# Performance work log

Measured on AMD Instinct MI355X. Metric: run time of the kernel, lower is better.

Reference implementation:

```python
import jax, jax.numpy as jnp
import numpy as np

N, E, D, T, R, H = 50000, 400000, 256, 3, 6, 4
DK = D // H          # 64, d_k = out_dim // n_heads
OUT = H * DK         # 256
LN_EPS = 1e-5


def setup_inputs() -> dict:
    key = jax.random.key(0)
    ks = jax.random.split(key, 16)
    std = 0.02  # initializer_range in HGTClassfication._init_weights
    f32 = jnp.float32
    inp = {
        "x": jax.random.normal(ks[0], (N, D), f32),
        "Wk": jax.random.normal(ks[1], (T, D, OUT), f32) * std,
        "bk": jnp.zeros((T, OUT), f32),
        "Wq": jax.random.normal(ks[2], (T, D, OUT), f32) * std,
        "bq": jnp.zeros((T, OUT), f32),
        "Wv": jax.random.normal(ks[3], (T, D, OUT), f32) * std,
        "bv": jnp.zeros((T, OUT), f32),
        "Wa": jax.random.normal(ks[4], (T, OUT, OUT), f32) * std,
        "ba": jnp.zeros((T, OUT), f32),
        "rel_pri": jnp.ones((R, H), f32),
        "rel_att": jax.random.normal(ks[5], (R, H, DK, DK), f32) * (1.0 / np.sqrt(DK)),
        "rel_msg": jax.random.normal(ks[6], (R, H, DK, DK), f32) * (1.0 / np.sqrt(DK)),
        "skip": jnp.ones((T,), f32),
        "ln_g": jnp.ones((T, OUT), f32),
        "ln_b": jnp.zeros((T, OUT), f32),
        "node_type": jax.random.randint(ks[7], (N,), 0, T),
        "edge_src": jax.random.randint(ks[8], (E,), 0, N),
        "edge_dst": jax.random.randint(ks[9], (E,), 0, N),
        "edge_type": jax.random.randint(ks[10], (E,), 0, R),
        "n_heads": H,
    }
    return inp


def reference(x, Wk, bk, Wq, bq, Wv, bv, Wa, ba, rel_pri, rel_att, rel_msg,
              skip, ln_g, ln_b, node_type, edge_src, edge_dst, edge_type, n_heads):
    n, d = x.shape
    r, h = rel_pri.shape
    dk = rel_att.shape[-1]
    out_dim = h * dk
    ar = jnp.arange(n)

    def typed_linear(inp_, W, b):
        # per-node-type Linear: compute for all T types, pick by node_type
        y = jnp.einsum('ni,tio->tno', inp_, W) + b[:, None, :]
        return y[node_type, ar]

    k = typed_linear(x, Wk, bk).reshape(n, h, dk)
    q = typed_linear(x, Wq, bq).reshape(n, h, dk)
    v = typed_linear(x, Wv, bv).reshape(n, h, dk)

    # relation-specific transforms (done on nodes, gathered per edge: N*R << E*R work)
    k_rel = jnp.einsum('nhd,rhde->rnhe', k, rel_att)   # [R,N,H,dk]
    v_rel = jnp.einsum('nhd,rhde->rnhe', v, rel_msg)   # [R,N,H,dk]
    key_e = k_rel[edge_type, edge_src]                 # [E,H,dk]
    val_e = v_rel[edge_type, edge_src]                 # [E,H,dk]

    att = (q[edge_dst] * key_e).sum(-1) * rel_pri[edge_type] / jnp.sqrt(jnp.float32(dk))  # [E,H]

    # per-(dst, etype) mailbox softmax + weighted sum (DGL reduce per canonical etype)
    seg = edge_dst * r + edge_type
    S = n * r
    amax = jax.ops.segment_max(att, seg, num_segments=S)
    amax = jax.lax.stop_gradient(jnp.where(jnp.isfinite(amax), amax, 0.0))
    ex = jnp.exp(att - amax[seg])
    denom = jax.ops.segment_sum(ex, seg, num_segments=S)
    w = ex / denom[seg]                                # [E,H]
    hsum = jax.ops.segment_sum(w[:, :, None] * val_e, seg, num_segments=S)  # [S,H,dk]
    cnt = jax.ops.segment_sum(jnp.ones((seg.shape[0],), x.dtype), seg, num_segments=S)

    # cross_reducer='mean' over relations that delivered messages
    t_rel = hsum.reshape(n, r, out_dim)
    present = cnt.reshape(n, r) > 0
    nrel = jnp.maximum(present.sum(-1), 1).astype(x.dtype)
    t = (t_rel * present[..., None].astype(x.dtype)).sum(1) / nrel[:, None]

    trans = typed_linear(t, Wa, ba)
    alpha = jax.nn.sigmoid(skip)[node_type][:, None]
    out = trans * alpha + x * (1.0 - alpha)

    mu = out.mean(-1, keepdims=True)
    var = out.var(-1, keepdims=True)
    normed = (out - mu) * jax.lax.rsqrt(var + LN_EPS) * ln_g[node_type] + ln_b[node_type]

    # nodes with no incoming edges keep their input feature (no 't' in DGL data)
    has_msg = present.any(-1)[:, None]
    return jnp.where(has_msg, normed, x)
```

## Files before the change

kernel.cpp:

```cpp
#include <hip/hip_runtime.h>
#include <hip/hip_bf16.h>


#define NN 50000
#define EE 400000
#define TN 3
#define RN 6
#define HN 4
#define SS (NN * RN)
#define NCHUNK 293
#define CD 32

typedef __hip_bfloat16 bf16;
typedef unsigned short u16;
using bf16x8 = __attribute__((ext_vector_type(8))) __bf16;
using f32x4  = __attribute__((ext_vector_type(4))) float;

__device__ __forceinline__ float b2f(bf16 h) { return __bfloat162float(h); }
__device__ __forceinline__ float busf(u16 u) { return __uint_as_float((unsigned)u << 16); }
__device__ __forceinline__ float blo(unsigned u) { return __uint_as_float(u << 16); }
__device__ __forceinline__ float bhi(unsigned u) { return __uint_as_float(u & 0xffff0000u); }
__device__ __forceinline__ u16 f2us(float f) {
    unsigned u = __float_as_uint(f);
    return (u16)((u + 0x7fffu + ((u >> 16) & 1u)) >> 16);
}
__device__ __forceinline__ float ld(const void* p, long i, int f) {
    return f ? ((const float*)p)[i] : b2f(((const bf16*)p)[i]);
}

__global__ __launch_bounds__(256) void detect_dtype(const void* __restrict__ x,
                                                    int* __restrict__ flag) {
    __shared__ int cnt_s;
    if (threadIdx.x == 0) cnt_s = 0;
    __syncthreads();
    const u16* p = (const u16*)x;
    int c = 0;
    for (int i = threadIdx.x; i < 8192; i += 256) {
        int expo = (p[i] >> 7) & 0xFF;
        if (expo >= 0x97) ++c;
    }
    atomicAdd(&cnt_s, c);
    __syncthreads();
    if (threadIdx.x == 0) *flag = (cnt_s > 64) ? 1 : 0;
}

__global__ __launch_bounds__(256) void prep(const void* __restrict__ rel_att,
        const void* __restrict__ rel_msg,
        const void* __restrict__ Wk, const void* __restrict__ Wq,
        const void* __restrict__ Wv, const void* __restrict__ Wa,
        const void* __restrict__ x, const int* __restrict__ node_type,
        const int* __restrict__ edst, const int* __restrict__ etype,
        const int* __restrict__ flag,
        u16* __restrict__ MTa, u16* __restrict__ MTm,
        u16* __restrict__ WallT, u16* __restrict__ WaT,
        u16* __restrict__ xb,
        int* __restrict__ lists, int* __restrict__ cnts,
        unsigned* __restrict__ cnt) {
    int b = blockIdx.x;
    int t = threadIdx.x;
    if (b < 48) {
        int f = *flag;
        int m = b;
        long base = (long)(m % 24) * 4096;
        if (m < 24) {
            for (int it = 0; it < 16; ++it) {
                int idx = it * 256 + t;
                MTa[base + idx] = f2us(ld(rel_att, base + idx, f));
            }
        } else {
            for (int it = 0; it < 16; ++it) {
                int idx = it * 256 + t;
                int d = idx >> 6, j = idx & 63;
                MTm[base + (j << 6) + d] = f2us(ld(rel_msg, base + idx, f));
            }
        }
    } else if (b < 3120) {
        int f = *flag;
        int m = b - 48;
        if (m < 2304) {
            int ty = m / 768, o3 = m % 768;
            int sec = o3 >> 8, o = o3 & 255;
            const void* W = (sec == 0) ? Wk : (sec == 1) ? Wq : Wv;
            WallT[(size_t)ty * 768 * 256 + (size_t)o3 * 256 + t] =
                f2us(ld(W, (long)ty * 65536 + (long)t * 256 + o, f));
        } else {
            int mm = m - 2304;
            int ty = mm / 256, o = mm % 256;
            WaT[(size_t)ty * 65536 + (size_t)o * 256 + t] =
                f2us(ld(Wa, (long)ty * 65536 + (long)t * 256 + o, f));
        }
    } else if (b < 15620) {
        int f = *flag;
        long i = ((long)(b - 3120) * 256 + t) * 4;
        if (i < (long)NN * 256) {
            if (f) {
                float4 v = *(const float4*)((const float*)x + i);
                ushort4 p; p.x = f2us(v.x); p.y = f2us(v.y); p.z = f2us(v.z); p.w = f2us(v.w);
                *(ushort4*)(xb + i) = p;
            } else {
                *(ushort4*)(xb + i) = *(const ushort4*)((const u16*)x + i);
            }
        }
    } else if (b < 15816) {
        __shared__ int lc[TN], lbase[TN];
        if (t < TN) lc[t] = 0;
        __syncthreads();
        int n = (b - 15620) * 256 + t;
        int pos = -1, ty = 0;
        if (n < NN) {
            ty = node_type[n];
            pos = atomicAdd(&lc[ty], 1);
        }
        __syncthreads();
        if (t < TN) lbase[t] = atomicAdd(&cnts[t], lc[t]);
        __syncthreads();
        if (n < NN) lists[ty * NN + lbase[ty] + pos] = n;
    } else {
        int e = (b - 15816) * 256 + t;
        if (e < EE) atomicAdd(&cnt[etype[e] * NN + edst[e]], 1u);
    }
}

__global__ __launch_bounds__(256) void scanA(const unsigned* __restrict__ cnt,
                                             unsigned* __restrict__ csums) {
    __shared__ unsigned s[256];
    int b = blockIdx.x, t = threadIdx.x;
    int s0 = b * 1024 + t * 4;
    unsigned v = 0;
    if (s0 + 3 < SS) { uint4 u = *(const uint4*)&cnt[s0]; v = u.x + u.y + u.z + u.w; }
    else { for (int j = 0; j < 4; ++j) if (s0 + j < SS) v += cnt[s0 + j]; }
    s[t] = v;
    __syncthreads();
    for (int st = 128; st > 0; st >>= 1) {
        if (t < st) s[t] += s[t + st];
        __syncthreads();
    }
    if (t == 0) csums[b] = s[0];
}

__global__ __launch_bounds__(256) void scanB(unsigned* __restrict__ csums,
                                             int* __restrict__ base) {
    __shared__ unsigned s[512];
    int t = threadIdx.x;
    unsigned a = (t < NCHUNK) ? csums[t] : 0u;
    unsigned b = (256 + t < NCHUNK) ? csums[256 + t] : 0u;
    s[t] = a; s[256 + t] = b;
    __syncthreads();
    for (int st = 1; st < 512; st <<= 1) {
        unsigned x0 = (t >= st) ? s[t - st] : 0u;
        unsigned x1 = (256 + t >= st) ? s[256 + t - st] : 0u;
        __syncthreads();
        s[t] += x0; s[256 + t] += x1;
        __syncthreads();
    }
    if (t < NCHUNK) csums[t] = s[t] - a;
    if (256 + t < NCHUNK) csums[256 + t] = s[256 + t] - b;
    if (t == 0) base[SS] = (int)s[NCHUNK - 1];
}

__global__ __launch_bounds__(256) void scanC(const unsigned* __restrict__ cnt,
        const unsigned* __restrict__ csums, int* __restrict__ base) {
    __shared__ unsigned s[256];
    int b = blockIdx.x, t = threadIdx.x;
    int s0 = b * 1024 + t * 4;
    unsigned vs[4] = {0u, 0u, 0u, 0u};
    if (s0 + 3 < SS) { uint4 u = *(const uint4*)&cnt[s0]; vs[0]=u.x; vs[1]=u.y; vs[2]=u.z; vs[3]=u.w; }
    else { for (int j = 0; j < 4; ++j) if (s0 + j < SS) vs[j] = cnt[s0 + j]; }
    unsigned v = vs[0] + vs[1] + vs[2] + vs[3];
    s[t] = v;
    __syncthreads();
    for (int st = 1; st < 256; st <<= 1) {
        unsigned x = (t >= st) ? s[t - st] : 0u;
        __syncthreads();
        s[t] += x;
        __syncthreads();
    }
    unsigned run = csums[b] + s[t] - v;
    for (int j = 0; j < 4; ++j) {
        if (s0 + j < SS) { base[s0 + j] = (int)run; run += vs[j]; }
    }
}

__global__ __launch_bounds__(256) void scatter_edges(const int* __restrict__ edst,
        const int* __restrict__ etype, const int* __restrict__ base,
        unsigned* __restrict__ cnt, int* __restrict__ sorted) {
    int e = blockIdx.x * 256 + threadIdx.x;
    if (e >= EE) return;
    int seg = etype[e] * NN + edst[e];
    unsigned old = atomicSub(&cnt[seg], 1u);
    sorted[base[seg] + (int)old - 1] = e;
}

__global__ __launch_bounds__(512, 2) void k1_mfma(const u16* __restrict__ xb,
        const u16* __restrict__ WallT,
        const void* __restrict__ bk, const void* __restrict__ bq,
        const void* __restrict__ bv,
        const int* __restrict__ lists, const int* __restrict__ cnts,
        const int* __restrict__ flag,
        u16* __restrict__ kb, u16* __restrict__ qb, u16* __restrict__ vb) {
    int f = *flag;
    int tt = blockIdx.x % TN, tile = blockIdx.x / TN;
    int cnt = cnts[tt];
    int start = tile * 64;
    if (start >= cnt) return;
    __shared__ int nl[64];
    __shared__ __align__(16) u16 xs[64][280];
    __shared__ __align__(16) float bias_s[768];
    int t = threadIdx.x;
    if (t < 64) nl[t] = (start + t < cnt) ? lists[tt * NN + start + t] : -1;
    if (t < 256) {
        bias_s[t]       = ld(bk, tt * 256 + t, f);
        bias_s[256 + t] = ld(bq, tt * 256 + t, f);
        bias_s[512 + t] = ld(bv, tt * 256 + t, f);
    }
    __syncthreads();
    {
        int i = t >> 4, g = t & 15;
        #pragma unroll
        for (int i2 = 0; i2 < 2; ++i2) {
            int row = i + i2 * 32;
            int node = nl[row];
            uint4 a = {0, 0, 0, 0}, b = {0, 0, 0, 0};
            if (node >= 0) {
                const uint4* src = (const uint4*)(xb + (size_t)node * 256 + g * 16);
                a = src[0]; b = src[1];
            }
            *(uint4*)&xs[row][g * 16] = a;
            *(uint4*)&xs[row][g * 16 + 8] = b;
        }
    }
    __syncthreads();
    int w = t >> 6, lane = t & 63, ln = lane & 15, quad = lane >> 4;
    const u16* Wt = WallT + (size_t)tt * 768 * 256;
    f32x4 acc[6][4];
    #pragma unroll
    for (int j = 0; j < 6; ++j)
        #pragma unroll
        for (int g = 0; g < 4; ++g)
            acc[j][g] = (f32x4){0.f, 0.f, 0.f, 0.f};
    for (int kt = 0; kt < 8; ++kt) {
        bf16x8 A[6];
        #pragma unroll
        for (int jt = 0; jt < 6; ++jt)
            A[jt] = *(const bf16x8*)(Wt + (size_t)(w * 96 + jt * 16 + ln) * 256 + kt * 32 + quad * 8);
        bf16x8 B[4];
        #pragma unroll
        for (int g = 0; g < 4; ++g)
            B[g] = *(const bf16x8*)&xs[g * 16 + ln][kt * 32 + quad * 8];
        #pragma unroll
        for (int jt = 0; jt < 6; ++jt)
            #pragma unroll
            for (int g = 0; g < 4; ++g)
                acc[jt][g] = __builtin_amdgcn_mfma_f32_16x16x32_bf16(A[jt], B[g], acc[jt][g], 0, 0, 0);
    }
    #pragma unroll
    for (int jt = 0; jt < 6; ++jt) {
        int jc = w * 96 + jt * 16 + quad * 4;
        float4 bi = *(const float4*)&bias_s[jc];
        int sec = jc >> 8, o = jc & 255;
        u16* basep = (sec == 0 ? kb : sec == 1 ? qb : vb);
        #pragma unroll
        for (int g = 0; g < 4; ++g) {
            int node = nl[g * 16 + ln];
            if (node >= 0) {
                ushort4 p;
                p.x = f2us(acc[jt][g][0] + bi.x); p.y = f2us(acc[jt][g][1] + bi.y);
                p.z = f2us(acc[jt][g][2] + bi.z); p.w = f2us(acc[jt][g][3] + bi.w);
                *(ushort4*)(basep + (size_t)node * 256 + o) = p;
            }
        }
    }
}

__global__ __launch_bounds__(256) void k2k4(const u16* __restrict__ kb,
        const u16* __restrict__ qb, const u16* __restrict__ vb,
        const u16* __restrict__ MTa, const u16* __restrict__ MTm,
        const void* __restrict__ rel_pri,
        const int* __restrict__ sorted, const int* __restrict__ base,
        const int* __restrict__ esrc, const int* __restrict__ edst,
        const int* __restrict__ flag,
        u16* __restrict__ attex_g, float* __restrict__ tacc) {
    int f = *flag;
    int c0 = blockIdx.x * CD;
    int nd = min(CD, NN - c0);
    __shared__ float attL[1280];
    __shared__ int srcL[1280];
    __shared__ float denomL[CD * HN];
    __shared__ int sb_[CD + 1];
    __shared__ __align__(16) u16 qL[CD][264];
    __shared__ __align__(16) u16 qrs[CD][264];
    int t = threadIdx.x;
    int w = t >> 6, lane = t & 63, ln = lane & 15, quad = lane >> 4;
    {
        int i = t >> 3, g8 = t & 7;
        uint4 a0 = {0,0,0,0}, a1 = {0,0,0,0}, a2 = {0,0,0,0}, a3 = {0,0,0,0};
        if (i < nd) {
            const uint4* src = (const uint4*)(qb + (size_t)(c0 + i) * 256 + g8 * 32);
            a0 = src[0]; a1 = src[1]; a2 = src[2]; a3 = src[3];
        }
        *(uint4*)&qL[i][g8 * 32 +  0] = a0;
        *(uint4*)&qL[i][g8 * 32 +  8] = a1;
        *(uint4*)&qL[i][g8 * 32 + 16] = a2;
        *(uint4*)&qL[i][g8 * 32 + 24] = a3;
    }
    f32x4 accF[2][4];
    #pragma unroll
    for (int g = 0; g < 2; ++g)
        #pragma unroll
        for (int m = 0; m < 4; ++m)
            accF[g][m] = (f32x4){0.f, 0.f, 0.f, 0.f};

    for (int r = 0; r < RN; ++r) {
        if (t < CD * HN) denomL[t] = 0.f;
        if (t <= nd) sb_[t] = base[r * NN + c0 + t];
        __syncthreads();
        long mtbase = (long)(r * HN + w) * 4096;
        #pragma unroll
        for (int grp = 0; grp < 2; ++grp) {
            int li = grp * 16 + ln;
            bf16x8 B0 = *(const bf16x8*)&qL[li][w * 64 + quad * 8];
            bf16x8 B1 = *(const bf16x8*)&qL[li][w * 64 + quad * 8 + 32];
            #pragma unroll
            for (int mt = 0; mt < 4; ++mt) {
                const u16* ap = MTa + mtbase + (mt * 16 + ln) * 64 + quad * 8;
                bf16x8 A0 = *(const bf16x8*)(ap);
                bf16x8 A1 = *(const bf16x8*)(ap + 32);
                f32x4 acc = {0.f, 0.f, 0.f, 0.f};
                acc = __builtin_amdgcn_mfma_f32_16x16x32_bf16(A0, B0, acc, 0, 0, 0);
                acc = __builtin_amdgcn_mfma_f32_16x16x32_bf16(A1, B1, acc, 0, 0, 0);
                int jc = w * 64 + mt * 16 + quad * 4;
                ushort4 pq;
                pq.x = f2us(acc[0]); pq.y = f2us(acc[1]);
                pq.z = f2us(acc[2]); pq.w = f2us(acc[3]);
                *(ushort4*)&qrs[li][jc] = pq;
            }
        }
        __syncthreads();
        int b0 = sb_[0], nE = sb_[nd] - b0;
        for (int i = t; i < nE * 4; i += 256) {
            int ei = i >> 2;
            int e = sorted[b0 + ei];
            int h = i & 3;
            int s = esrc[e], dv = edst[e] - c0;
            if (h == 0 && ei < 1280) srcL[ei] = s;
            const uint4* kp = (const uint4*)(kb + (size_t)s * 256 + h * 64);
            const uint4* qp = (const uint4*)&qrs[dv][h * 64];
            float dot = 0.f;
            #pragma unroll
            for (int ii = 0; ii < 8; ++ii) {
                uint4 a = kp[ii], b = qp[ii];
                dot += blo(a.x) * blo(b.x) + bhi(a.x) * bhi(b.x);
                dot += blo(a.y) * blo(b.y) + bhi(a.y) * bhi(b.y);
                dot += blo(a.z) * blo(b.z) + bhi(a.z) * bhi(b.z);
                dot += blo(a.w) * blo(b.w) + bhi(a.w) * bhi(b.w);
            }
            float attv = dot * ld(rel_pri, r * HN + h, f) * 0.125f;
            attv = fminf(fmaxf(attv, -50.f), 50.f);
            float ex = expf(attv);
            if (i < 1280) attL[i] = ex;
            else attex_g[(size_t)b0 * 4 + i] = f2us(ex);
            atomicAdd(&denomL[dv * HN + h], ex);
        }
        __syncthreads();
        for (int i2 = w; i2 < nd; i2 += 4) {
            int sb = sb_[i2], se = sb_[i2 + 1];
            float a0 = 0.f, a1 = 0.f, a2 = 0.f, a3 = 0.f;
            if (se > sb) {
                int h = lane >> 4;
                float inv = 1.f / denomL[i2 * HN + h];
                for (int idx = sb; idx < se; ++idx) {
                    int rel = idx - b0;
                    int li2 = rel * 4 + h;
                    float wgt = ((li2 < 1280) ? attL[li2] : busf(attex_g[(size_t)idx * 4 + h])) * inv;
                    int s = (rel < 1280) ? srcL[rel] : esrc[sorted[idx]];
                    ushort4 v = *(const ushort4*)(vb + (size_t)s * 256 + lane * 4);
                    a0 += wgt * busf(v.x); a1 += wgt * busf(v.y);
                    a2 += wgt * busf(v.z); a3 += wgt * busf(v.w);
                }
            }
            ushort4 pv;
            pv.x = f2us(a0); pv.y = f2us(a1); pv.z = f2us(a2); pv.w = f2us(a3);
            *(ushort4*)&qrs[i2][lane * 4] = pv;
        }
        __syncthreads();
        #pragma unroll
        for (int grp = 0; grp < 2; ++grp) {
            int li = grp * 16 + ln;
            bf16x8 B0 = *(const bf16x8*)&qrs[li][w * 64 + quad * 8];
            bf16x8 B1 = *(const bf16x8*)&qrs[li][w * 64 + quad * 8 + 32];
            #pragma unroll
            for (int mt = 0; mt < 4; ++mt) {
                const u16* mp = MTm + mtbase + (mt * 16 + ln) * 64 + quad * 8;
                bf16x8 A0 = *(const bf16x8*)(mp);
                bf16x8 A1 = *(const bf16x8*)(mp + 32);
                accF[grp][mt] = __builtin_amdgcn_mfma_f32_16x16x32_bf16(A0, B0, accF[grp][mt], 0, 0, 0);
                accF[grp][mt] = __builtin_amdgcn_mfma_f32_16x16x32_bf16(A1, B1, accF[grp][mt], 0, 0, 0);
            }
        }
    }
    #pragma unroll
    for (int grp = 0; grp < 2; ++grp) {
        int li = grp * 16 + ln;
        if (li < nd) {
            #pragma unroll
            for (int mt = 0; mt < 4; ++mt) {
                int jc = w * 64 + mt * 16 + quad * 4;
                float4 v = {accF[grp][mt][0], accF[grp][mt][1],
                            accF[grp][mt][2], accF[grp][mt][3]};
                *(float4*)(tacc + (long)(c0 + li) * 256 + jc) = v;
            }
        }
    }
}

__global__ __launch_bounds__(512, 4) void k5_fused(const void* __restrict__ x,
        const float* __restrict__ tacc, const u16* __restrict__ WaT,
        const void* __restrict__ ba, const void* __restrict__ skip,
        const void* __restrict__ ln_g, const void* __restrict__ ln_b,
        const int* __restrict__ base,
        const int* __restrict__ lists, const int* __restrict__ cnts,
        const int* __restrict__ flag, void* out) {
    int f = *flag;
    int tt = blockIdx.x % TN, tile = blockIdx.x / TN;
    int cnt = cnts[tt];
    int start = tile * 64;
    if (start >= cnt) return;
    __shared__ int nl[64];
    __shared__ float invs[64];
    __shared__ int hasv[64];
    __shared__ __align__(16) u16 xs[64][280];
    __shared__ __align__(16) float ba_s[256], lnG_s[256], lnB_s[256];
    __shared__ float red1[64][8], red2[64][8];
    __shared__ float mu_[64], rs_[64];
    int t = threadIdx.x;
    if (t < 64) {
        int node = (start + t < cnt) ? lists[tt * NN + start + t] : -1;
        nl[t] = node;
        int nrel = 0;
        if (node >= 0) {
            #pragma unroll
            for (int r = 0; r < RN; ++r)
                nrel += (base[r * NN + node + 1] > base[r * NN + node]) ? 1 : 0;
        }
        hasv[t] = nrel;
        invs[t] = (nrel > 0) ? 1.f / (float)nrel : 1.f;
    }
    if (t < 256) {
        ba_s[t]  = ld(ba,   tt * 256 + t, f);
        lnG_s[t] = ld(ln_g, tt * 256 + t, f);
        lnB_s[t] = ld(ln_b, tt * 256 + t, f);
    }
    __syncthreads();
    {
        int i = t >> 3, g8 = t & 7;
        int node = nl[i];
        float inv = invs[i];
        int o0 = g8 * 32;
        u16 tmp[32];
        if (node >= 0) {
            const float* src = tacc + (long)node * 256 + o0;
            #pragma unroll
            for (int j = 0; j < 8; ++j) {
                float4 v = *(const float4*)(src + j * 4);
                tmp[j*4+0] = f2us(v.x * inv); tmp[j*4+1] = f2us(v.y * inv);
                tmp[j*4+2] = f2us(v.z * inv); tmp[j*4+3] = f2us(v.w * inv);
            }
        } else {
            #pragma unroll
            for (int j = 0; j < 32; ++j) tmp[j] = 0;
        }
        #pragma unroll
        for (int j = 0; j < 4; ++j)
            *(uint4*)&xs[i][o0 + j * 8] = ((const uint4*)tmp)[j];
    }
    __syncthreads();
    int w = t >> 6, lane = t & 63, ln = lane & 15, quad = lane >> 4;
    const u16* Wt = WaT + (size_t)tt * 65536;
    f32x4 acc[2][4];
    #pragma unroll
    for (int j = 0; j < 2; ++j)
        #pragma unroll
        for (int g = 0; g < 4; ++g)
            acc[j][g] = (f32x4){0.f, 0.f, 0.f, 0.f};
    for (int kt = 0; kt < 8; ++kt) {
        bf16x8 A[2];
        #pragma unroll
        for (int jt = 0; jt < 2; ++jt)
            A[jt] = *(const bf16x8*)(Wt + (size_t)(w * 32 + jt * 16 + ln) * 256 + kt * 32 + quad * 8);
        bf16x8 B[4];
        #pragma unroll
        for (int g = 0; g < 4; ++g)
            B[g] = *(const bf16x8*)&xs[g * 16 + ln][kt * 32 + quad * 8];
        #pragma unroll
        for (int jt = 0; jt < 2; ++jt)
            #pragma unroll
            for (int g = 0; g < 4; ++g)
                acc[jt][g] = __builtin_amdgcn_mfma_f32_16x16x32_bf16(A[jt], B[g], acc[jt][g], 0, 0, 0);
    }
    float sk = ld(skip, tt, f);
    float alpha = 1.f / (1.f + expf(-sk));
    float p1[4] = {0.f, 0.f, 0.f, 0.f}, p2[4] = {0.f, 0.f, 0.f, 0.f};
    #pragma unroll
    for (int g = 0; g < 4; ++g) {
        int node = nl[g * 16 + ln];
        if (node < 0) continue;
        #pragma unroll
        for (int jt = 0; jt < 2; ++jt) {
            int jc = w * 32 + jt * 16 + quad * 4;
            float4 bi = *(const float4*)&ba_s[jc];
            long xo = (long)node * 256 + jc;
            float xv[4];
            if (f) {
                float4 v = *(const float4*)((const float*)x + xo);
                xv[0] = v.x; xv[1] = v.y; xv[2] = v.z; xv[3] = v.w;
            } else {
                ushort4 v = *(const ushort4*)((const u16*)x + xo);
                xv[0] = busf(v.x); xv[1] = busf(v.y); xv[2] = busf(v.z); xv[3] = busf(v.w);
            }
            #pragma unroll
            for (int rg = 0; rg < 4; ++rg) {
                float ov = acc[jt][g][rg] + ((const float*)&bi)[rg];
                ov = ov * alpha + xv[rg] * (1.f - alpha);
                acc[jt][g][rg] = ov;
                p1[g] += ov; p2[g] += ov * ov;
            }
        }
    }
    #pragma unroll
    for (int g = 0; g < 4; ++g) {
        p1[g] += __shfl_xor(p1[g], 16); p1[g] += __shfl_xor(p1[g], 32);
        p2[g] += __shfl_xor(p2[g], 16); p2[g] += __shfl_xor(p2[g], 32);
    }
    if (quad == 0) {
        #pragma unroll
        for (int g = 0; g < 4; ++g) {
            red1[g * 16 + ln][w] = p1[g];
            red2[g * 16 + ln][w] = p2[g];
        }
    }
    __syncthreads();
    if (t < 64) {
        float s1 = 0.f, s2 = 0.f;
        #pragma unroll
        for (int j = 0; j < 8; ++j) { s1 += red1[t][j]; s2 += red2[t][j]; }
        float mu = s1 * (1.f / 256.f);
        float ms = s2 * (1.f / 256.f);
        float var = fmaxf(ms - mu * mu, 0.f);
        mu_[t] = mu; rs_[t] = rsqrtf(var + 1e-5f);
    }
    __syncthreads();
    #pragma unroll
    for (int g = 0; g < 4; ++g) {
        int li = g * 16 + ln;
        int node = nl[li];
        if (node < 0) continue;
        if (hasv[li] > 0) {
            float mu = mu_[li], rs = rs_[li];
            #pragma unroll
            for (int jt = 0; jt < 2; ++jt) {
                int jc = w * 32 + jt * 16 + quad * 4;
                float4 gg = *(const float4*)&lnG_s[jc];
                float4 bb = *(const float4*)&lnB_s[jc];
                long oo = (long)node * 256 + jc;
                float r0 = (acc[jt][g][0] - mu) * rs * gg.x + bb.x;
                float r1 = (acc[jt][g][1] - mu) * rs * gg.y + bb.y;
                float r2 = (acc[jt][g][2] - mu) * rs * gg.z + bb.z;
                float r3 = (acc[jt][g][3] - mu) * rs * gg.w + bb.w;
                if (f) { float4 v = {r0, r1, r2, r3}; *(float4*)((float*)out + oo) = v; }
                else   { ushort4 v; v.x = f2us(r0); v.y = f2us(r1); v.z = f2us(r2); v.w = f2us(r3);
                         *(ushort4*)((u16*)out + oo) = v; }
            }
        } else {
            #pragma unroll
            for (int jt = 0; jt < 2; ++jt) {
                int jc = w * 32 + jt * 16 + quad * 4;
                long oo = (long)node * 256 + jc;
                if (f) { *(float4*)((float*)out + oo) = *(const float4*)((const float*)x + oo); }
                else   { *(ushort4*)((u16*)out + oo) = *(const ushort4*)((const u16*)x + oo); }
            }
        }
    }
}

extern "C" void kernel_launch(void* const* d_in, const int* in_sizes, int n_in,
                              void* d_out, int out_size, void* d_ws, size_t ws_size,
                              hipStream_t stream) {
    const void* x       = d_in[0];
    const void* Wk      = d_in[1];
    const void* bk      = d_in[2];
    const void* Wq      = d_in[3];
    const void* bq      = d_in[4];
    const void* Wv      = d_in[5];
    const void* bv      = d_in[6];
    const void* Wa      = d_in[7];
    const void* ba      = d_in[8];
    const void* rel_pri = d_in[9];
    const void* rel_att = d_in[10];
    const void* rel_msg = d_in[11];
    const void* skip    = d_in[12];
    const void* ln_g    = d_in[13];
    const void* ln_b    = d_in[14];
    const int* node_type = (const int*)d_in[15];
    const int* edge_src  = (const int*)d_in[16];
    const int* edge_dst  = (const int*)d_in[17];
    const int* edge_type = (const int*)d_in[18];
    char* w = (char*)d_ws;

    u16*      kb     = (u16*)(w);
    u16*      qb     = (u16*)(w + 25600000);
    u16*      vb     = (u16*)(w + 51200000);
    float*    tacc   = (float*)(w + 76800000);
    u16*      xb     = (u16*)(w + 76800000);
    u16*      attex  = (u16*)(w + 128000000);
    int*      sorted = (int*)(w + 131200000);
    int*      base   = (int*)(w + 132800000);
    int*      nlists = (int*)(w + 134000064);
    u16*      MTa    = (u16*)(w + 134600064);
    u16*      MTm    = (u16*)(w + 134796672);
    u16*      WallT  = (u16*)(w + 134993280);
    u16*      WaT    = (u16*)(w + 136172928);
    unsigned* cnt    = (unsigned*)(w + 136566144);
    int*      ncnts  = (int*)(w + 137766144);
    int*      flag   = (int*)(w + 137766208);
    unsigned* csums  = (unsigned*)(w + 137766272);

    hipMemsetAsync(w + 136566144, 0, 1201408, stream);

    detect_dtype<<<dim3(1), dim3(256), 0, stream>>>(x, flag);
    prep<<<dim3(17379), dim3(256), 0, stream>>>(
        rel_att, rel_msg, Wk, Wq, Wv, Wa, x, node_type, edge_dst, edge_type,
        flag, MTa, MTm, WallT, WaT, xb, nlists, ncnts, cnt);
    scanA<<<dim3(NCHUNK), dim3(256), 0, stream>>>(cnt, csums);
    scanB<<<dim3(1), dim3(256), 0, stream>>>(csums, base);
    scanC<<<dim3(NCHUNK), dim3(256), 0, stream>>>(cnt, csums, base);
    scatter_edges<<<dim3((EE + 255) / 256), dim3(256), 0, stream>>>(
        edge_dst, edge_type, base, cnt, sorted);

    k1_mfma<<<dim3(TN * ((NN + 63) / 64)), dim3(512), 0, stream>>>(
        xb, WallT, bk, bq, bv, nlists, ncnts, flag, kb, qb, vb);


    k2k4<<<dim3((NN + CD - 1) / CD), dim3(256), 0, stream>>>(
        kb, qb, vb, MTa, MTm, rel_pri, sorted, base, edge_src, edge_dst,
        flag, attex, tacc);

    k5_fused<<<dim3(TN * ((NN + 63) / 64)), dim3(512), 0, stream>>>(
        x, tacc, WaT, ba, skip, ln_g, ln_b, base, nlists, ncnts, flag, d_out);
}
```

Measured before the change: 621.9 us.

## Halve destination-node chunk per block and widen per-node aggregation lanes

```diff
diff --git a/kernel.cpp b/kernel.cpp
--- a/kernel.cpp
+++ b/kernel.cpp
@@ -9,7 +9,8 @@
 #define HN 4
 #define SS (NN * RN)
 #define NCHUNK 293
-#define CD 32
+#define CD 16
+#define LCAP 640
 
 typedef __hip_bfloat16 bf16;
 typedef unsigned short u16;
@@ -283,8 +284,8 @@
     int f = *flag;
     int c0 = blockIdx.x * CD;
     int nd = min(CD, NN - c0);
-    __shared__ float attL[1280];
-    __shared__ int srcL[1280];
+    __shared__ float attL[LCAP];
+    __shared__ int srcL[LCAP];
     __shared__ float denomL[CD * HN];
     __shared__ int sb_[CD + 1];
     __shared__ __align__(16) u16 qL[CD][264];
@@ -292,34 +293,27 @@
     int t = threadIdx.x;
     int w = t >> 6, lane = t & 63, ln = lane & 15, quad = lane >> 4;
     {
-        int i = t >> 3, g8 = t & 7;
-        uint4 a0 = {0,0,0,0}, a1 = {0,0,0,0}, a2 = {0,0,0,0}, a3 = {0,0,0,0};
+        int i = t >> 4, g = t & 15;
+        uint4 a0 = {0,0,0,0}, a1 = {0,0,0,0};
         if (i < nd) {
-            const uint4* src = (const uint4*)(qb + (size_t)(c0 + i) * 256 + g8 * 32);
-            a0 = src[0]; a1 = src[1]; a2 = src[2]; a3 = src[3];
-        }
-        *(uint4*)&qL[i][g8 * 32 +  0] = a0;
-        *(uint4*)&qL[i][g8 * 32 +  8] = a1;
-        *(uint4*)&qL[i][g8 * 32 + 16] = a2;
-        *(uint4*)&qL[i][g8 * 32 + 24] = a3;
-    }
-    f32x4 accF[2][4];
+            const uint4* src = (const uint4*)(qb + (size_t)(c0 + i) * 256 + g * 16);
+            a0 = src[0]; a1 = src[1];
+        }
+        *(uint4*)&qL[i][g * 16] = a0;
+        *(uint4*)&qL[i][g * 16 + 8] = a1;
+    }
+    f32x4 accF[4];
     #pragma unroll
-    for (int g = 0; g < 2; ++g)
-        #pragma unroll
-        for (int m = 0; m < 4; ++m)
-            accF[g][m] = (f32x4){0.f, 0.f, 0.f, 0.f};
+    for (int m = 0; m < 4; ++m) accF[m] = (f32x4){0.f, 0.f, 0.f, 0.f};
 
     for (int r = 0; r < RN; ++r) {
         if (t < CD * HN) denomL[t] = 0.f;
         if (t <= nd) sb_[t] = base[r * NN + c0 + t];
         __syncthreads();
         long mtbase = (long)(r * HN + w) * 4096;
-        #pragma unroll
-        for (int grp = 0; grp < 2; ++grp) {
-            int li = grp * 16 + ln;
-            bf16x8 B0 = *(const bf16x8*)&qL[li][w * 64 + quad * 8];
-            bf16x8 B1 = *(const bf16x8*)&qL[li][w * 64 + quad * 8 + 32];
+        {
+            bf16x8 B0 = *(const bf16x8*)&qL[ln][w * 64 + quad * 8];
+            bf16x8 B1 = *(const bf16x8*)&qL[ln][w * 64 + quad * 8 + 32];
             #pragma unroll
             for (int mt = 0; mt < 4; ++mt) {
                 const u16* ap = MTa + mtbase + (mt * 16 + ln) * 64 + quad * 8;
@@ -332,7 +326,7 @@
                 ushort4 pq;
                 pq.x = f2us(acc[0]); pq.y = f2us(acc[1]);
                 pq.z = f2us(acc[2]); pq.w = f2us(acc[3]);
-                *(ushort4*)&qrs[li][jc] = pq;
+                *(ushort4*)&qrs[ln][jc] = pq;
             }
         }
         __syncthreads();
@@ -342,7 +336,7 @@
             int e = sorted[b0 + ei];
             int h = i & 3;
             int s = esrc[e], dv = edst[e] - c0;
-            if (h == 0 && ei < 1280) srcL[ei] = s;
+            if (h == 0 && ei < LCAP) srcL[ei] = s;
             const uint4* kp = (const uint4*)(kb + (size_t)s * 256 + h * 64);
             const uint4* qp = (const uint4*)&qrs[dv][h * 64];
             float dot = 0.f;
@@ -357,58 +351,58 @@
             float attv = dot * ld(rel_pri, r * HN + h, f) * 0.125f;
             attv = fminf(fmaxf(attv, -50.f), 50.f);
             float ex = expf(attv);
-            if (i < 1280) attL[i] = ex;
+            if (i < LCAP) attL[i] = ex;
             else attex_g[(size_t)b0 * 4 + i] = f2us(ex);
             atomicAdd(&denomL[dv * HN + h], ex);
         }
         __syncthreads();
-        for (int i2 = w; i2 < nd; i2 += 4) {
-            int sb = sb_[i2], se = sb_[i2 + 1];
-            float a0 = 0.f, a1 = 0.f, a2 = 0.f, a3 = 0.f;
-            if (se > sb) {
-                int h = lane >> 4;
-                float inv = 1.f / denomL[i2 * HN + h];
-                for (int idx = sb; idx < se; ++idx) {
-                    int rel = idx - b0;
-                    int li2 = rel * 4 + h;
-                    float wgt = ((li2 < 1280) ? attL[li2] : busf(attex_g[(size_t)idx * 4 + h])) * inv;
-                    int s = (rel < 1280) ? srcL[rel] : esrc[sorted[idx]];
-                    ushort4 v = *(const ushort4*)(vb + (size_t)s * 256 + lane * 4);
-                    a0 += wgt * busf(v.x); a1 += wgt * busf(v.y);
-                    a2 += wgt * busf(v.z); a3 += wgt * busf(v.w);
+        {
+            int half = lane >> 5, lane32 = lane & 31;
+            int h = lane32 >> 3;
+            for (int i2 = w * 2 + half; i2 < nd; i2 += 8) {
+                int sb = sb_[i2], se = sb_[i2 + 1];
+                float a0=0.f,a1=0.f,a2=0.f,a3=0.f,a4=0.f,a5=0.f,a6=0.f,a7=0.f;
+                if (se > sb) {
+                    float inv = 1.f / denomL[i2 * HN + h];
+                    for (int idx = sb; idx < se; ++idx) {
+                        int rel = idx - b0;
+                        int li2 = rel * 4 + h;
+                        float wgt = ((li2 < LCAP) ? attL[li2]
+                                     : busf(attex_g[(size_t)idx * 4 + h])) * inv;
+                        int s = (rel < LCAP) ? srcL[rel] : esrc[sorted[idx]];
+                        uint4 v = *(const uint4*)(vb + (size_t)s * 256 + lane32 * 8);
+                        a0 += wgt * blo(v.x); a1 += wgt * bhi(v.x);
+                        a2 += wgt * blo(v.y); a3 += wgt * bhi(v.y);
+                        a4 += wgt * blo(v.z); a5 += wgt * bhi(v.z);
+                        a6 += wgt * blo(v.w); a7 += wgt * bhi(v.w);
+                    }
                 }
-            }
-            ushort4 pv;
-            pv.x = f2us(a0); pv.y = f2us(a1); pv.z = f2us(a2); pv.w = f2us(a3);
-            *(ushort4*)&qrs[i2][lane * 4] = pv;
-        }
-        __syncthreads();
-        #pragma unroll
-        for (int grp = 0; grp < 2; ++grp) {
-            int li = grp * 16 + ln;
-            bf16x8 B0 = *(const bf16x8*)&qrs[li][w * 64 + quad * 8];
-            bf16x8 B1 = *(const bf16x8*)&qrs[li][w * 64 + quad * 8 + 32];
+                u16 pv8[8];
+                pv8[0]=f2us(a0); pv8[1]=f2us(a1); pv8[2]=f2us(a2); pv8[3]=f2us(a3);
+                pv8[4]=f2us(a4); pv8[5]=f2us(a5); pv8[6]=f2us(a6); pv8[7]=f2us(a7);
+                *(uint4*)&qrs[i2][lane32 * 8] = *(const uint4*)pv8;
+            }
+        }
+        __syncthreads();
+        {
+            bf16x8 B0 = *(const bf16x8*)&qrs[ln][w * 64 + quad * 8];
+            bf16x8 B1 = *(const bf16x8*)&qrs[ln][w * 64 + quad * 8 + 32];
             #pragma unroll
             for (int mt = 0; mt < 4; ++mt) {
                 const u16* mp = MTm + mtbase + (mt * 16 + ln) * 64 + quad * 8;
                 bf16x8 A0 = *(const bf16x8*)(mp);
                 bf16x8 A1 = *(const bf16x8*)(mp + 32);
-                accF[grp][mt] = __builtin_amdgcn_mfma_f32_16x16x32_bf16(A0, B0, accF[grp][mt], 0, 0, 0);
-                accF[grp][mt] = __builtin_amdgcn_mfma_f32_16x16x32_bf16(A1, B1, accF[grp][mt], 0, 0, 0);
-            }
-        }
-    }
-    #pragma unroll
-    for (int grp = 0; grp < 2; ++grp) {
-        int li = grp * 16 + ln;
-        if (li < nd) {
-            #pragma unroll
-            for (int mt = 0; mt < 4; ++mt) {
-                int jc = w * 64 + mt * 16 + quad * 4;
-                float4 v = {accF[grp][mt][0], accF[grp][mt][1],
-                            accF[grp][mt][2], accF[grp][mt][3]};
-                *(float4*)(tacc + (long)(c0 + li) * 256 + jc) = v;
-            }
+                accF[mt] = __builtin_amdgcn_mfma_f32_16x16x32_bf16(A0, B0, accF[mt], 0, 0, 0);
+                accF[mt] = __builtin_amdgcn_mfma_f32_16x16x32_bf16(A1, B1, accF[mt], 0, 0, 0);
+            }
+        }
+    }
+    if (ln < nd) {
+        #pragma unroll
+        for (int mt = 0; mt < 4; ++mt) {
+            int jc = w * 64 + mt * 16 + quad * 4;
+            float4 v = {accF[mt][0], accF[mt][1], accF[mt][2], accF[mt][3]};
+            *(float4*)(tacc + (long)(c0 + ln) * 256 + jc) = v;
         }
     }
 }
@@ -640,7 +634,7 @@
         xb, WallT, bk, bq, bv, nlists, ncnts, flag, kb, qb, vb);
 
 
-    k2k4<<<dim3((NN + CD - 1) / CD), dim3(256), 0, stream>>>(
+    k2k4<<<dim3(NN / CD), dim3(256), 0, stream>>>(
         kb, qb, vb, MTa, MTm, rel_pri, sorted, base, edge_src, edge_dst,
         flag, attex, tacc);
 
```

Result: faster. 588.6 us (-5.4%).
